# Optimization experiments

Hardware: AMD Instinct MI355X
Metric: run time of the kernel (lower is better)

Reference implementation:

```python
import jax, jax.numpy as jnp
import numpy as np

LATENT = 2048
PROJ = 128
N = 4096
TEMP = 0.5
BN_EPS = 1e-5
COS_EPS = 1e-8


def _batchnorm(x, gamma=None, beta=None):
    # training-mode BatchNorm1d: biased batch stats
    mean = jnp.mean(x, axis=0)
    var = jnp.mean((x - mean) ** 2, axis=0)
    xn = (x - mean) * jax.lax.rsqrt(var + BN_EPS)
    if gamma is not None:
        xn = xn * gamma + beta
    return xn


def _project(h, W1, gamma1, beta1, W2):
    x = h @ W1.T                      # [N, latent]
    x = jax.nn.relu(_batchnorm(x, gamma1, beta1))
    x = x @ W2.T                      # [N, proj]
    return _batchnorm(x)              # bn2 affine=False


def _normalize(z):
    n = jnp.linalg.norm(z, axis=-1, keepdims=True)
    return z / jnp.maximum(n, COS_EPS)


def setup_inputs() -> dict:
    key = jax.random.key(0)
    ks = jax.random.split(key, 4)
    scale_w1 = 1.0 / np.sqrt(LATENT)
    return {
        "h1": jax.random.normal(ks[0], (N, LATENT), jnp.float32),
        "h2": jax.random.normal(ks[1], (N, LATENT), jnp.float32),
        "W1": jax.random.normal(ks[2], (LATENT, LATENT), jnp.float32) * scale_w1,
        "gamma1": jnp.ones((LATENT,), jnp.float32),
        "beta1": jnp.zeros((LATENT,), jnp.float32),
        "W2": jax.random.normal(ks[3], (PROJ, LATENT), jnp.float32) * scale_w1,
    }


def reference(h1, h2, W1, gamma1, beta1, W2):
    z1 = _project(h1, W1, gamma1, beta1, W2)
    z2 = _project(h2, W1, gamma1, beta1, W2)
    zn1 = _normalize(z1)
    zn2 = _normalize(z2)
    inv_t = 1.0 / TEMP
    # cosine similarity as normalized GEMMs (same math as broadcast cossim)
    sim11 = (zn1 @ zn1.T) * inv_t      # [N, N]
    sim22 = (zn2 @ zn2.T) * inv_t
    sim12 = (zn1 @ zn2.T) * inv_t
    d = sim12.shape[-1]
    eye = jnp.eye(d, dtype=bool)
    neg_inf = jnp.float32(-jnp.inf)
    sim11 = jnp.where(eye, neg_inf, sim11)
    sim22 = jnp.where(eye, neg_inf, sim22)
    raw_scores1 = jnp.concatenate([sim12, sim11], axis=-1)       # [N, 2N]
    raw_scores2 = jnp.concatenate([sim22, sim12.T], axis=-1)     # [N, 2N]
    raw_scores = jnp.concatenate([raw_scores1, raw_scores2], axis=-2)  # [2N, 2N]
    targets = jnp.arange(2 * d, dtype=jnp.int64 if jax.config.jax_enable_x64 else jnp.int32)
    return raw_scores, targets
```

## Files before the change

### kernel.cpp

```cpp
#include <hip/hip_runtime.h>
#include <hip/hip_bf16.h>
#include <math.h>

#define NROWS 4096
#define MTOT  8192
#define LATENT 2048
#define PROJ 128
#define OUTN 8192
#define SPLITK 8
#define CH2 128

using bf16 = __hip_bfloat16;
using bf16x8 = __attribute__((ext_vector_type(8))) short;
using bf16x4 = __attribute__((ext_vector_type(4))) short;
using f32x4  = __attribute__((ext_vector_type(4))) float;

#define LDS_AS(p) ((__attribute__((address_space(3))) void*)(p))
#define GLB_AS(p) ((const __attribute__((address_space(1))) void*)(p))

__device__ __forceinline__ float bf2f(short s) {
    return __uint_as_float(((unsigned)(unsigned short)s) << 16);
}
__device__ __forceinline__ short f2bf(float f) {
    bf16 h = __float2bfloat16(f);
    return __builtin_bit_cast(short, h);
}

__global__ void conv_all(const float* __restrict__ W1, const float* __restrict__ W2,
                         const float* __restrict__ h1, const float* __restrict__ h2,
                         bf16* __restrict__ W1b, bf16* __restrict__ W2b,
                         bf16* __restrict__ hb)
{
    const size_t g = ((size_t)blockIdx.x * 256 + threadIdx.x) * 8;
    const size_t N_W1 = (size_t)LATENT * LATENT;
    const size_t N_W2 = (size_t)PROJ * LATENT;
    const size_t N_H  = (size_t)NROWS * LATENT;
    const float* src; bf16* dst; size_t off;
    if (g < N_W1)                  { src = W1; dst = W1b;       off = g; }
    else if (g < N_W1 + N_W2)      { src = W2; dst = W2b;       off = g - N_W1; }
    else if (g < N_W1 + N_W2 + N_H){ src = h1; dst = hb;        off = g - N_W1 - N_W2; }
    else                           { src = h2; dst = hb + N_H;  off = g - N_W1 - N_W2 - N_H; }
    const float4 v0 = *reinterpret_cast<const float4*>(src + off);
    const float4 v1 = *reinterpret_cast<const float4*>(src + off + 4);
    bf16x8 o;
    o[0] = f2bf(v0.x); o[1] = f2bf(v0.y); o[2] = f2bf(v0.z); o[3] = f2bf(v0.w);
    o[4] = f2bf(v1.x); o[5] = f2bf(v1.y); o[6] = f2bf(v1.z); o[7] = f2bf(v1.w);
    *reinterpret_cast<bf16x8*>(dst + off) = o;
}

#define AREG(buf,kh) (sm + ((buf)*2 + (kh)) * 16384)
#define BREG(buf,kh) (sm + 65536 + ((buf)*2 + (kh)) * 16384)

#define LDA_(buf,kh,m) (*reinterpret_cast<const bf16x8*>(AREG(buf,kh) + (wr*128 + (m)*16 + fr)*64 + rslot))
#define LDB_(buf,kh,n) (*reinterpret_cast<const bf16x8*>(BREG(buf,kh) + (wc*64  + (n)*16 + fr)*64 + rslot))

#define STAGE_A(buf,kh,kt) do { \
    const bf16* g_ = Ag + (size_t)(bm + w*16 + srow) * 2048 + (kt)*64 + (kh)*32 + selem; \
    __builtin_amdgcn_global_load_lds(GLB_AS(g_),                  LDS_AS(AREG(buf,kh) + w*1024),        16, 0, 0); \
    __builtin_amdgcn_global_load_lds(GLB_AS(g_ + (size_t)128*2048), LDS_AS(AREG(buf,kh) + 8192 + w*1024), 16, 0, 0); \
} while(0)

#define STAGE_B(buf,kh,kt) do { \
    const bf16* g_ = Bg + (size_t)(bn + w*16 + srow) * 2048 + (kt)*64 + (kh)*32 + selem; \
    __builtin_amdgcn_global_load_lds(GLB_AS(g_),                  LDS_AS(BREG(buf,kh) + w*1024),        16, 0, 0); \
    __builtin_amdgcn_global_load_lds(GLB_AS(g_ + (size_t)128*2048), LDS_AS(BREG(buf,kh) + 8192 + w*1024), 16, 0, 0); \
} while(0)

#define PH(bufi, khi, mb, READB, STAGE_STMT, DO_VMCNT) do { \
    if (READB) { b0 = LDB_(bufi,khi,0); b1 = LDB_(bufi,khi,1); b2 = LDB_(bufi,khi,2); b3 = LDB_(bufi,khi,3); } \
    bf16x8 a0 = LDA_(bufi,khi,(mb)+0), a1 = LDA_(bufi,khi,(mb)+1), a2 = LDA_(bufi,khi,(mb)+2), a3 = LDA_(bufi,khi,(mb)+3); \
    STAGE_STMT; \
    __builtin_amdgcn_s_barrier(); \
    asm volatile("s_waitcnt lgkmcnt(0)" ::: "memory"); \
    __builtin_amdgcn_sched_barrier(0); \
    __builtin_amdgcn_s_setprio(1); \
    acc[(mb)+0][0] = __builtin_amdgcn_mfma_f32_16x16x32_bf16(b0, a0, acc[(mb)+0][0], 0,0,0); \
    acc[(mb)+0][1] = __builtin_amdgcn_mfma_f32_16x16x32_bf16(b1, a0, acc[(mb)+0][1], 0,0,0); \
    acc[(mb)+0][2] = __builtin_amdgcn_mfma_f32_16x16x32_bf16(b2, a0, acc[(mb)+0][2], 0,0,0); \
    acc[(mb)+0][3] = __builtin_amdgcn_mfma_f32_16x16x32_bf16(b3, a0, acc[(mb)+0][3], 0,0,0); \
    acc[(mb)+1][0] = __builtin_amdgcn_mfma_f32_16x16x32_bf16(b0, a1, acc[(mb)+1][0], 0,0,0); \
    acc[(mb)+1][1] = __builtin_amdgcn_mfma_f32_16x16x32_bf16(b1, a1, acc[(mb)+1][1], 0,0,0); \
    acc[(mb)+1][2] = __builtin_amdgcn_mfma_f32_16x16x32_bf16(b2, a1, acc[(mb)+1][2], 0,0,0); \
    acc[(mb)+1][3] = __builtin_amdgcn_mfma_f32_16x16x32_bf16(b3, a1, acc[(mb)+1][3], 0,0,0); \
    acc[(mb)+2][0] = __builtin_amdgcn_mfma_f32_16x16x32_bf16(b0, a2, acc[(mb)+2][0], 0,0,0); \
    acc[(mb)+2][1] = __builtin_amdgcn_mfma_f32_16x16x32_bf16(b1, a2, acc[(mb)+2][1], 0,0,0); \
    acc[(mb)+2][2] = __builtin_amdgcn_mfma_f32_16x16x32_bf16(b2, a2, acc[(mb)+2][2], 0,0,0); \
    acc[(mb)+2][3] = __builtin_amdgcn_mfma_f32_16x16x32_bf16(b3, a2, acc[(mb)+2][3], 0,0,0); \
    acc[(mb)+3][0] = __builtin_amdgcn_mfma_f32_16x16x32_bf16(b0, a3, acc[(mb)+3][0], 0,0,0); \
    acc[(mb)+3][1] = __builtin_amdgcn_mfma_f32_16x16x32_bf16(b1, a3, acc[(mb)+3][1], 0,0,0); \
    acc[(mb)+3][2] = __builtin_amdgcn_mfma_f32_16x16x32_bf16(b2, a3, acc[(mb)+3][2], 0,0,0); \
    acc[(mb)+3][3] = __builtin_amdgcn_mfma_f32_16x16x32_bf16(b3, a3, acc[(mb)+3][3], 0,0,0); \
    __builtin_amdgcn_s_setprio(0); \
    if (DO_VMCNT) { asm volatile("s_waitcnt vmcnt(6)" ::: "memory"); } \
    __builtin_amdgcn_s_barrier(); \
    __builtin_amdgcn_sched_barrier(0); \
} while (0)

__global__ __launch_bounds__(512, 2)
void gemm1_256(const bf16* __restrict__ Ag, const bf16* __restrict__ Bg,
               bf16* __restrict__ C, float* __restrict__ pS1, float* __restrict__ pSS1)
{
    extern __shared__ __align__(16) char sm[];

    const int t    = threadIdx.x;
    const int lane = t & 63;
    const int w    = t >> 6;
    const int wr   = w >> 2;
    const int wc   = w & 3;

    const int bid = blockIdx.x;
    const int lin = (bid & 7) * 32 + (bid >> 3);
    const int bm  = (lin >> 3) * 256;
    const int bn  = (lin & 7) * 256;

    const int srow  = lane >> 2;
    const int selem = 8 * ((lane & 3) ^ ((lane >> 2) & 3));
    const int fr    = lane & 15;
    const int rslot = 16 * ((lane >> 4) ^ (lane & 3));

    f32x4 acc[8][4];
#pragma unroll
    for (int m = 0; m < 8; ++m)
#pragma unroll
        for (int n = 0; n < 4; ++n)
#pragma unroll
            for (int r = 0; r < 4; ++r) acc[m][n][r] = 0.f;

    bf16x8 b0, b1, b2, b3;

    STAGE_B(0,0,0); STAGE_A(0,0,0); STAGE_B(0,1,0); STAGE_A(0,1,0);
    STAGE_B(1,0,1); STAGE_A(1,0,1); STAGE_B(1,1,1);
    asm volatile("s_waitcnt vmcnt(6)" ::: "memory");
    __builtin_amdgcn_s_barrier();
    __builtin_amdgcn_sched_barrier(0);

    for (int i = 0; i < 15; ++i) {
        const int kt1 = 2*i + 1, kt2 = 2*i + 2, kt3 = 2*i + 3;
        PH(0,0, 0, true,  STAGE_A(1,1,kt1), false);
        PH(0,0, 4, false, STAGE_B(0,0,kt2), false);
        PH(0,1, 0, true,  STAGE_A(0,0,kt2), false);
        PH(0,1, 4, false, STAGE_B(0,1,kt2), true);
        PH(1,0, 0, true,  STAGE_A(0,1,kt2), false);
        PH(1,0, 4, false, STAGE_B(1,0,kt3), false);
        PH(1,1, 0, true,  STAGE_A(1,0,kt3), false);
        PH(1,1, 4, false, STAGE_B(1,1,kt3), true);
    }

    STAGE_A(1,1,31);
    asm volatile("s_waitcnt vmcnt(0)" ::: "memory");
    __builtin_amdgcn_s_barrier();
    __builtin_amdgcn_sched_barrier(0);
    PH(0,0, 0, true,  ((void)0), false);
    PH(0,0, 4, false, ((void)0), false);
    PH(0,1, 0, true,  ((void)0), false);
    PH(0,1, 4, false, ((void)0), false);
    PH(1,0, 0, true,  ((void)0), false);
    PH(1,0, 4, false, ((void)0), false);
    PH(1,1, 0, true,  ((void)0), false);
    PH(1,1, 4, false, ((void)0), false);

    const int j_l = (lane >> 4) * 4;
#pragma unroll
    for (int m = 0; m < 8; ++m)
#pragma unroll
        for (int n = 0; n < 4; ++n) {
            const int crow = bm + wr * 128 + m * 16 + fr;
            const int ccol = bn + wc * 64 + n * 16 + j_l;
            bf16x4 o;
#pragma unroll
            for (int r = 0; r < 4; ++r) o[r] = f2bf(acc[m][n][r]);
            *reinterpret_cast<bf16x4*>(&C[(size_t)crow * LATENT + ccol]) = o;
        }

#pragma unroll
    for (int n = 0; n < 4; ++n)
#pragma unroll
        for (int r = 0; r < 4; ++r) {
            float sv = 0.f, qv = 0.f;
#pragma unroll
            for (int m = 0; m < 8; ++m) {
                const float v = acc[m][n][r];
                sv += v;
                qv = fmaf(v, v, qv);
            }
#pragma unroll
            for (int o = 1; o < 16; o <<= 1) {
                sv += __shfl_xor(sv, o);
                qv += __shfl_xor(qv, o);
            }
            if (fr == 0) {
                const int slot = ((bm >> 8) << 1) + wr;
                const int col  = bn + wc * 64 + n * 16 + j_l + r;
                pS1 [(size_t)slot * LATENT + col] = sv;
                pSS1[(size_t)slot * LATENT + col] = qv;
            }
        }
}

__global__ void stats1_final(const float* __restrict__ pS, const float* __restrict__ pSS,
                             float* __restrict__ mean, float* __restrict__ rstd)
{
    const int c    = blockIdx.x * 256 + threadIdx.x;
    const int half = blockIdx.y;
    float s = 0.f, ss = 0.f;
    for (int i = 0; i < 32; ++i) {
        s  += pS [((size_t)(half * 32 + i)) * LATENT + c];
        ss += pSS[((size_t)(half * 32 + i)) * LATENT + c];
    }
    const float m   = s / NROWS;
    const float var = ss / NROWS - m * m;
    mean[half * LATENT + c] = m;
    rstd[half * LATENT + c] = 1.0f / sqrtf(var + 1e-5f);
}

__global__ void bn1_apply_relu_bf16(bf16* __restrict__ X,
                                    const float* __restrict__ mean, const float* __restrict__ rstd,
                                    const float* __restrict__ gamma, const float* __restrict__ beta)
{
    const size_t idx = (size_t)blockIdx.x * 256 + threadIdx.x;
    const size_t e   = idx * 8;
    const int c      = (int)(e & (LATENT - 1));
    const int half   = (int)(e >> 23);
    const int sc     = half * LATENT + c;
    const bf16x8 v = *reinterpret_cast<const bf16x8*>(X + e);
    const float4 m0 = *reinterpret_cast<const float4*>(mean + sc);
    const float4 m1 = *reinterpret_cast<const float4*>(mean + sc + 4);
    const float4 r0 = *reinterpret_cast<const float4*>(rstd + sc);
    const float4 r1 = *reinterpret_cast<const float4*>(rstd + sc + 4);
    const float4 g0 = *reinterpret_cast<const float4*>(gamma + c);
    const float4 g1 = *reinterpret_cast<const float4*>(gamma + c + 4);
    const float4 b0 = *reinterpret_cast<const float4*>(beta + c);
    const float4 b1 = *reinterpret_cast<const float4*>(beta + c + 4);
    const float mm[8] = {m0.x, m0.y, m0.z, m0.w, m1.x, m1.y, m1.z, m1.w};
    const float rr[8] = {r0.x, r0.y, r0.z, r0.w, r1.x, r1.y, r1.z, r1.w};
    const float gg[8] = {g0.x, g0.y, g0.z, g0.w, g1.x, g1.y, g1.z, g1.w};
    const float bb[8] = {b0.x, b0.y, b0.z, b0.w, b1.x, b1.y, b1.z, b1.w};
    bf16x8 o;
#pragma unroll
    for (int j = 0; j < 8; ++j) {
        const float f = fmaxf(fmaf((bf2f(v[j]) - mm[j]) * rr[j], gg[j], bb[j]), 0.f);
        o[j] = f2bf(f);
    }
    *reinterpret_cast<bf16x8*>(X + e) = o;
}

__global__ __launch_bounds__(256)
void gemm2_splitk(const bf16* __restrict__ A, const bf16* __restrict__ B,
                  float* __restrict__ Part)
{
    __shared__ __align__(16) bf16 As[128 * 32];
    __shared__ __align__(16) bf16 Bs[128 * 32];

    const int kc = blockIdx.x;
    const int bm = blockIdx.y * 128;

    const int t    = threadIdx.x;
    const int lane = t & 63;
    const int w    = t >> 6;
    const int wr   = w >> 1;
    const int wc   = w & 1;
    const int lrow = lane >> 2;
    const int lcol = (lane & 3) * 8;

    f32x4 acc[4][4];
#pragma unroll
    for (int m = 0; m < 4; ++m)
#pragma unroll
        for (int n = 0; n < 4; ++n)
#pragma unroll
            for (int r = 0; r < 4; ++r) acc[m][n][r] = 0.f;

    const int fr = lane & 15;
    const int fk = (lane >> 4) * 8;
    const int kbeg = kc * (LATENT / SPLITK);
    const int kend = kbeg + (LATENT / SPLITK);

    for (int k0 = kbeg; k0 < kend; k0 += 32) {
#pragma unroll
        for (int q = 0; q < 2; ++q) {
            const int chunk = w * 2 + q;
            const int row = chunk * 16 + lrow;
            __builtin_amdgcn_global_load_lds(
                GLB_AS(&A[(size_t)(bm + row) * LATENT + k0 + lcol]),
                LDS_AS(&As[chunk * 512]), 16, 0, 0);
            __builtin_amdgcn_global_load_lds(
                GLB_AS(&B[(size_t)row * LATENT + k0 + lcol]),
                LDS_AS(&Bs[chunk * 512]), 16, 0, 0);
        }
        __syncthreads();

        bf16x8 a[4], b[4];
#pragma unroll
        for (int m = 0; m < 4; ++m)
            a[m] = *reinterpret_cast<const bf16x8*>(&As[(wr * 64 + m * 16 + fr) * 32 + fk]);
#pragma unroll
        for (int n = 0; n < 4; ++n)
            b[n] = *reinterpret_cast<const bf16x8*>(&Bs[(wc * 64 + n * 16 + fr) * 32 + fk]);

#pragma unroll
        for (int m = 0; m < 4; ++m)
#pragma unroll
            for (int n = 0; n < 4; ++n)
                acc[m][n] = __builtin_amdgcn_mfma_f32_16x16x32_bf16(b[n], a[m], acc[m][n], 0, 0, 0);
        __syncthreads();
    }

    const int i_l = lane & 15;
    const int j_l = (lane >> 4) * 4;
#pragma unroll
    for (int m = 0; m < 4; ++m)
#pragma unroll
        for (int n = 0; n < 4; ++n) {
            const int crow = bm + wr * 64 + m * 16 + i_l;
            const int ccol = wc * 64 + n * 16 + j_l;
            *reinterpret_cast<float4*>(&Part[((size_t)kc * MTOT + crow) * PROJ + ccol]) =
                make_float4(acc[m][n][0], acc[m][n][1], acc[m][n][2], acc[m][n][3]);
        }
}

__global__ __launch_bounds__(128)
void reduce2_kern(const float* __restrict__ Part, float* __restrict__ Z,
                  float* __restrict__ pS2, float* __restrict__ pSS2)
{
    const int c     = threadIdx.x;
    const int chunk = blockIdx.x;
    const int r0    = chunk * (MTOT / CH2);
    float s = 0.f, ss = 0.f;
    for (int r = r0; r < r0 + MTOT / CH2; ++r) {
        float z = 0.f;
#pragma unroll
        for (int kc = 0; kc < SPLITK; ++kc)
            z += Part[((size_t)kc * MTOT + r) * PROJ + c];
        Z[(size_t)r * PROJ + c] = z;
        s += z;
        ss = fmaf(z, z, ss);
    }
    pS2 [(size_t)chunk * PROJ + c] = s;
    pSS2[(size_t)chunk * PROJ + c] = ss;
}

__global__ __launch_bounds__(128)
void stats2_final(const float* __restrict__ pS, const float* __restrict__ pSS,
                  float* __restrict__ mean, float* __restrict__ rstd)
{
    const int c    = threadIdx.x;
    const int half = blockIdx.x;
    float s = 0.f, ss = 0.f;
    for (int i = 0; i < CH2 / 2; ++i) {
        s  += pS [(size_t)(half * (CH2 / 2) + i) * PROJ + c];
        ss += pSS[(size_t)(half * (CH2 / 2) + i) * PROJ + c];
    }
    const float m   = s / NROWS;
    const float var = ss / NROWS - m * m;
    mean[half * PROJ + c] = m;
    rstd[half * PROJ + c] = 1.0f / sqrtf(var + 1e-5f);
}

__global__ __launch_bounds__(256)
void bn2_normalize_bf16(const float* __restrict__ Z,
                        const float* __restrict__ mean, const float* __restrict__ rstd,
                        bf16* __restrict__ Zn, int* __restrict__ tgt)
{
    const int row  = blockIdx.x * 4 + (threadIdx.x >> 6);
    const int half = row >> 12;
    const int lane = threadIdx.x & 63;
    const float* zr = Z + (size_t)row * PROJ;
    const float v0 = (zr[lane]      - mean[half * PROJ + lane])      * rstd[half * PROJ + lane];
    const float v1 = (zr[lane + 64] - mean[half * PROJ + lane + 64]) * rstd[half * PROJ + lane + 64];
    float ss = v0 * v0 + v1 * v1;
#pragma unroll
    for (int o = 32; o > 0; o >>= 1) ss += __shfl_xor(ss, o);
    const float inv = 1.0f / fmaxf(sqrtf(ss), 1e-8f);
    bf16* orow = Zn + (size_t)row * PROJ;
    orow[lane]      = __float2bfloat16(v0 * inv);
    orow[lane + 64] = __float2bfloat16(v1 * inv);
    if (lane == 0) tgt[row] = row;
}

__global__ __launch_bounds__(256)
void sim_bf16(const bf16* __restrict__ zn, float* __restrict__ out)
{
    __shared__ __align__(16) bf16 As[4 * 128 * 32];
    __shared__ __align__(16) bf16 Bs[4 * 128 * 32];

    const int t    = threadIdx.x;
    const int lane = t & 63;
    const int w    = t >> 6;
    const int wr   = w >> 1;
    const int wc   = w & 1;
    const int bi   = blockIdx.y * 128;
    const int bj   = blockIdx.x * 128;

    const bf16* Ub = zn + (size_t)bi * PROJ;
    const bf16* Vb = zn + (size_t)(bj ^ 4096) * PROJ;

    const int srow = t >> 2;
    const int ske  = (t & 3) * 8;

#pragma unroll
    for (int q = 0; q < 4; ++q)
#pragma unroll
        for (int h = 0; h < 2; ++h) {
            const int row = h * 64 + srow;
            const int ke  = q * 32 + ske;
            __builtin_amdgcn_global_load_lds(
                GLB_AS(&Ub[(size_t)row * PROJ + ke]),
                LDS_AS(&As[q * 4096 + h * 2048 + srow * 32 + ske]), 16, 0, 0);
            __builtin_amdgcn_global_load_lds(
                GLB_AS(&Vb[(size_t)row * PROJ + ke]),
                LDS_AS(&Bs[q * 4096 + h * 2048 + srow * 32 + ske]), 16, 0, 0);
        }
    __syncthreads();

    f32x4 acc[4][4];
#pragma unroll
    for (int m = 0; m < 4; ++m)
#pragma unroll
        for (int n = 0; n < 4; ++n)
#pragma unroll
            for (int r = 0; r < 4; ++r) acc[m][n][r] = 0.f;

    const int fr = lane & 15;
    const int fk = (lane >> 4) * 8;

#pragma unroll
    for (int q = 0; q < 4; ++q) {
        bf16x8 a[4], b[4];
#pragma unroll
        for (int m = 0; m < 4; ++m)
            a[m] = *reinterpret_cast<const bf16x8*>(&As[q * 4096 + (wr * 64 + m * 16 + fr) * 32 + fk]);
#pragma unroll
        for (int n = 0; n < 4; ++n)
            b[n] = *reinterpret_cast<const bf16x8*>(&Bs[q * 4096 + (wc * 64 + n * 16 + fr) * 32 + fk]);
#pragma unroll
        for (int m = 0; m < 4; ++m)
#pragma unroll
            for (int n = 0; n < 4; ++n)
                acc[m][n] = __builtin_amdgcn_mfma_f32_16x16x32_bf16(b[n], a[m], acc[m][n], 0, 0, 0);
    }

    const int i_l = lane & 15;
    const int j_l = (lane >> 4) * 4;
#pragma unroll
    for (int m = 0; m < 4; ++m)
#pragma unroll
        for (int n = 0; n < 4; ++n) {
            const int gi  = bi + wr * 64 + m * 16 + i_l;
            const int gj0 = bj + wc * 64 + n * 16 + j_l;
            f32x4 v;
#pragma unroll
            for (int r = 0; r < 4; ++r) v[r] = acc[m][n][r] * 2.0f;
            const int mj = (gi ^ 4096) - gj0;
            if (mj >= 0 && mj < 4) v[mj] = -1.0e30f;
            __builtin_nontemporal_store(
                v, reinterpret_cast<f32x4*>(&out[(size_t)gi * OUTN + gj0]));
        }
}

extern "C" void kernel_launch(void* const* d_in, const int* in_sizes, int n_in,
                              void* d_out, int out_size, void* d_ws, size_t ws_size,
                              hipStream_t stream)
{
    const float* h1 = (const float*)d_in[0];
    const float* h2 = (const float*)d_in[1];
    const float* W1 = (const float*)d_in[2];
    const float* g1 = (const float*)d_in[3];
    const float* b1 = (const float*)d_in[4];
    const float* W2 = (const float*)d_in[5];
    float* out = (float*)d_out;

    char* p = (char*)d_ws;
    auto carve = [&](size_t bytes) { char* r = p; p += (bytes + 255) & ~(size_t)255; return r; };
    bf16*  W1b   = (bf16*) carve((size_t)LATENT * LATENT * 2);
    bf16*  W2b   = (bf16*) carve((size_t)PROJ * LATENT * 2);
    bf16*  hb    = (bf16*) carve((size_t)MTOT * LATENT * 2);
    bf16*  X     = (bf16*) carve((size_t)MTOT * LATENT * 2);
    float* Part  = (float*)carve((size_t)SPLITK * MTOT * PROJ * 4);
    float* Z     = (float*)carve((size_t)MTOT * PROJ * 4);
    bf16*  znb   = (bf16*) carve((size_t)MTOT * PROJ * 2);
    float* pS1   = (float*)carve((size_t)64 * LATENT * 4);
    float* pSS1  = (float*)carve((size_t)64 * LATENT * 4);
    float* pS2   = (float*)carve((size_t)CH2 * PROJ * 4);
    float* pSS2  = (float*)carve((size_t)CH2 * PROJ * 4);
    float* mean1 = (float*)carve(2 * LATENT * 4);
    float* rstd1 = (float*)carve(2 * LATENT * 4);
    float* mean2 = (float*)carve(2 * PROJ * 4);
    float* rstd2 = (float*)carve(2 * PROJ * 4);

    const int conv_groups = (LATENT * LATENT + PROJ * LATENT + 2 * NROWS * LATENT) / 8;
    conv_all<<<dim3(conv_groups / 256), 256, 0, stream>>>(W1, W2, h1, h2, W1b, W2b, hb);

    gemm1_256<<<dim3(256), 512, 131072, stream>>>(hb, W1b, X, pS1, pSS1);

    stats1_final<<<dim3(LATENT / 256, 2), 256, 0, stream>>>(pS1, pSS1, mean1, rstd1);
    bn1_apply_relu_bf16<<<dim3(MTOT * LATENT / 2048), 256, 0, stream>>>(X, mean1, rstd1, g1, b1);

    gemm2_splitk<<<dim3(SPLITK, MTOT / 128), 256, 0, stream>>>(X, W2b, Part);
    reduce2_kern<<<dim3(CH2), 128, 0, stream>>>(Part, Z, pS2, pSS2);
    stats2_final<<<dim3(2), 128, 0, stream>>>(pS2, pSS2, mean2, rstd2);

    int* tgt = (int*)(out + (size_t)OUTN * OUTN);
    bn2_normalize_bf16<<<dim3(MTOT / 4), 256, 0, stream>>>(Z, mean2, rstd2, znb, tgt);

    sim_bf16<<<dim3(OUTN / 128, OUTN / 128), 256, 0, stream>>>(znb, out);
}
```

Measured before the change: 231.8 us.

## Fuse BN1 apply+ReLU into GEMM2 A-load and fold stats2 into normalize

```diff
diff --git a/kernel.cpp b/kernel.cpp
--- a/kernel.cpp
+++ b/kernel.cpp
@@ -198,7 +198,8 @@
 }
 
 __global__ void stats1_final(const float* __restrict__ pS, const float* __restrict__ pSS,
-                             float* __restrict__ mean, float* __restrict__ rstd)
+                             const float* __restrict__ gamma, const float* __restrict__ beta,
+                             float* __restrict__ scale1, float* __restrict__ shift1)
 {
     const int c    = blockIdx.x * 256 + threadIdx.x;
     const int half = blockIdx.y;
@@ -207,52 +208,25 @@
         s  += pS [((size_t)(half * 32 + i)) * LATENT + c];
         ss += pSS[((size_t)(half * 32 + i)) * LATENT + c];
     }
-    const float m   = s / NROWS;
-    const float var = ss / NROWS - m * m;
-    mean[half * LATENT + c] = m;
-    rstd[half * LATENT + c] = 1.0f / sqrtf(var + 1e-5f);
-}
-
-__global__ void bn1_apply_relu_bf16(bf16* __restrict__ X,
-                                    const float* __restrict__ mean, const float* __restrict__ rstd,
-                                    const float* __restrict__ gamma, const float* __restrict__ beta)
-{
-    const size_t idx = (size_t)blockIdx.x * 256 + threadIdx.x;
-    const size_t e   = idx * 8;
-    const int c      = (int)(e & (LATENT - 1));
-    const int half   = (int)(e >> 23);
-    const int sc     = half * LATENT + c;
-    const bf16x8 v = *reinterpret_cast<const bf16x8*>(X + e);
-    const float4 m0 = *reinterpret_cast<const float4*>(mean + sc);
-    const float4 m1 = *reinterpret_cast<const float4*>(mean + sc + 4);
-    const float4 r0 = *reinterpret_cast<const float4*>(rstd + sc);
-    const float4 r1 = *reinterpret_cast<const float4*>(rstd + sc + 4);
-    const float4 g0 = *reinterpret_cast<const float4*>(gamma + c);
-    const float4 g1 = *reinterpret_cast<const float4*>(gamma + c + 4);
-    const float4 b0 = *reinterpret_cast<const float4*>(beta + c);
-    const float4 b1 = *reinterpret_cast<const float4*>(beta + c + 4);
-    const float mm[8] = {m0.x, m0.y, m0.z, m0.w, m1.x, m1.y, m1.z, m1.w};
-    const float rr[8] = {r0.x, r0.y, r0.z, r0.w, r1.x, r1.y, r1.z, r1.w};
-    const float gg[8] = {g0.x, g0.y, g0.z, g0.w, g1.x, g1.y, g1.z, g1.w};
-    const float bb[8] = {b0.x, b0.y, b0.z, b0.w, b1.x, b1.y, b1.z, b1.w};
-    bf16x8 o;
-#pragma unroll
-    for (int j = 0; j < 8; ++j) {
-        const float f = fmaxf(fmaf((bf2f(v[j]) - mm[j]) * rr[j], gg[j], bb[j]), 0.f);
-        o[j] = f2bf(f);
-    }
-    *reinterpret_cast<bf16x8*>(X + e) = o;
+    const float m    = s / NROWS;
+    const float var  = ss / NROWS - m * m;
+    const float rstd = 1.0f / sqrtf(var + 1e-5f);
+    const float sc   = rstd * gamma[c];
+    scale1[half * LATENT + c] = sc;
+    shift1[half * LATENT + c] = beta[c] - m * sc;
 }
 
 __global__ __launch_bounds__(256)
-void gemm2_splitk(const bf16* __restrict__ A, const bf16* __restrict__ B,
-                  float* __restrict__ Part)
+void gemm2_fused(const bf16* __restrict__ A, const bf16* __restrict__ B,
+                 const float* __restrict__ scale1, const float* __restrict__ shift1,
+                 float* __restrict__ Part)
 {
     __shared__ __align__(16) bf16 As[128 * 32];
     __shared__ __align__(16) bf16 Bs[128 * 32];
 
     const int kc = blockIdx.x;
     const int bm = blockIdx.y * 128;
+    const int hb_ = (bm >> 12) * LATENT;
 
     const int t    = threadIdx.x;
     const int lane = t & 63;
@@ -281,11 +255,26 @@
             const int chunk = w * 2 + q;
             const int row = chunk * 16 + lrow;
             __builtin_amdgcn_global_load_lds(
-                GLB_AS(&A[(size_t)(bm + row) * LATENT + k0 + lcol]),
-                LDS_AS(&As[chunk * 512]), 16, 0, 0);
-            __builtin_amdgcn_global_load_lds(
                 GLB_AS(&B[(size_t)row * LATENT + k0 + lcol]),
                 LDS_AS(&Bs[chunk * 512]), 16, 0, 0);
+        }
+        const float4 sc0 = *reinterpret_cast<const float4*>(&scale1[hb_ + k0 + lcol]);
+        const float4 sc1 = *reinterpret_cast<const float4*>(&scale1[hb_ + k0 + lcol + 4]);
+        const float4 sh0 = *reinterpret_cast<const float4*>(&shift1[hb_ + k0 + lcol]);
+        const float4 sh1 = *reinterpret_cast<const float4*>(&shift1[hb_ + k0 + lcol + 4]);
+        const float scv[8] = {sc0.x, sc0.y, sc0.z, sc0.w, sc1.x, sc1.y, sc1.z, sc1.w};
+        const float shv[8] = {sh0.x, sh0.y, sh0.z, sh0.w, sh1.x, sh1.y, sh1.z, sh1.w};
+#pragma unroll
+        for (int q = 0; q < 2; ++q) {
+            const int chunk = w * 2 + q;
+            const int row = chunk * 16 + lrow;
+            const bf16x8 av = *reinterpret_cast<const bf16x8*>(
+                &A[(size_t)(bm + row) * LATENT + k0 + lcol]);
+            bf16x8 o;
+#pragma unroll
+            for (int j = 0; j < 8; ++j)
+                o[j] = f2bf(fmaxf(fmaf(bf2f(av[j]), scv[j], shv[j]), 0.f));
+            *reinterpret_cast<bf16x8*>(&As[chunk * 512 + lane * 8]) = o;
         }
         __syncthreads();
 
@@ -339,42 +328,49 @@
     pSS2[(size_t)chunk * PROJ + c] = ss;
 }
 
-__global__ __launch_bounds__(128)
-void stats2_final(const float* __restrict__ pS, const float* __restrict__ pSS,
-                  float* __restrict__ mean, float* __restrict__ rstd)
-{
-    const int c    = threadIdx.x;
-    const int half = blockIdx.x;
-    float s = 0.f, ss = 0.f;
-    for (int i = 0; i < CH2 / 2; ++i) {
-        s  += pS [(size_t)(half * (CH2 / 2) + i) * PROJ + c];
-        ss += pSS[(size_t)(half * (CH2 / 2) + i) * PROJ + c];
-    }
-    const float m   = s / NROWS;
-    const float var = ss / NROWS - m * m;
-    mean[half * PROJ + c] = m;
-    rstd[half * PROJ + c] = 1.0f / sqrtf(var + 1e-5f);
-}
-
 __global__ __launch_bounds__(256)
-void bn2_normalize_bf16(const float* __restrict__ Z,
-                        const float* __restrict__ mean, const float* __restrict__ rstd,
-                        bf16* __restrict__ Zn, int* __restrict__ tgt)
-{
-    const int row  = blockIdx.x * 4 + (threadIdx.x >> 6);
-    const int half = row >> 12;
-    const int lane = threadIdx.x & 63;
-    const float* zr = Z + (size_t)row * PROJ;
-    const float v0 = (zr[lane]      - mean[half * PROJ + lane])      * rstd[half * PROJ + lane];
-    const float v1 = (zr[lane + 64] - mean[half * PROJ + lane + 64]) * rstd[half * PROJ + lane + 64];
-    float ss = v0 * v0 + v1 * v1;
-#pragma unroll
-    for (int o = 32; o > 0; o >>= 1) ss += __shfl_xor(ss, o);
-    const float inv = 1.0f / fmaxf(sqrtf(ss), 1e-8f);
-    bf16* orow = Zn + (size_t)row * PROJ;
-    orow[lane]      = __float2bfloat16(v0 * inv);
-    orow[lane + 64] = __float2bfloat16(v1 * inv);
-    if (lane == 0) tgt[row] = row;
+void bn2_norm(const float* __restrict__ Z,
+              const float* __restrict__ pS2, const float* __restrict__ pSS2,
+              bf16* __restrict__ Zn, int* __restrict__ tgt)
+{
+    __shared__ float sm_mean[PROJ];
+    __shared__ float sm_rstd[PROJ];
+
+    const int blk  = blockIdx.x;
+    const int half = blk >> 5;
+    const int t    = threadIdx.x;
+
+    if (t < PROJ) {
+        float s = 0.f, ss = 0.f;
+        for (int i = 0; i < CH2 / 2; ++i) {
+            const int chunk = half * (CH2 / 2) + i;
+            s  += pS2 [(size_t)chunk * PROJ + t];
+            ss += pSS2[(size_t)chunk * PROJ + t];
+        }
+        const float m   = s / NROWS;
+        const float var = ss / NROWS - m * m;
+        sm_mean[t] = m;
+        sm_rstd[t] = 1.0f / sqrtf(var + 1e-5f);
+    }
+    __syncthreads();
+
+    const int lane = t & 63;
+    const int sub  = t >> 6;
+#pragma unroll 4
+    for (int it = 0; it < 32; ++it) {
+        const int row = blk * 128 + it * 4 + sub;
+        const float* zr = Z + (size_t)row * PROJ;
+        const float v0 = (zr[lane]      - sm_mean[lane])      * sm_rstd[lane];
+        const float v1 = (zr[lane + 64] - sm_mean[lane + 64]) * sm_rstd[lane + 64];
+        float ss = v0 * v0 + v1 * v1;
+#pragma unroll
+        for (int o = 32; o > 0; o >>= 1) ss += __shfl_xor(ss, o);
+        const float inv = 1.0f / fmaxf(sqrtf(ss), 1e-8f);
+        bf16* orow = Zn + (size_t)row * PROJ;
+        orow[lane]      = __float2bfloat16(v0 * inv);
+        orow[lane + 64] = __float2bfloat16(v1 * inv);
+        if (lane == 0) tgt[row] = row;
+    }
 }
 
 __global__ __launch_bounds__(256)
@@ -482,25 +478,22 @@
     float* pSS1  = (float*)carve((size_t)64 * LATENT * 4);
     float* pS2   = (float*)carve((size_t)CH2 * PROJ * 4);
     float* pSS2  = (float*)carve((size_t)CH2 * PROJ * 4);
-    float* mean1 = (float*)carve(2 * LATENT * 4);
-    float* rstd1 = (float*)carve(2 * LATENT * 4);
-    float* mean2 = (float*)carve(2 * PROJ * 4);
-    float* rstd2 = (float*)carve(2 * PROJ * 4);
+    float* scale1= (float*)carve(2 * LATENT * 4);
+    float* shift1= (float*)carve(2 * LATENT * 4);
 
     const int conv_groups = (LATENT * LATENT + PROJ * LATENT + 2 * NROWS * LATENT) / 8;
     conv_all<<<dim3(conv_groups / 256), 256, 0, stream>>>(W1, W2, h1, h2, W1b, W2b, hb);
 
     gemm1_256<<<dim3(256), 512, 131072, stream>>>(hb, W1b, X, pS1, pSS1);
 
-    stats1_final<<<dim3(LATENT / 256, 2), 256, 0, stream>>>(pS1, pSS1, mean1, rstd1);
-    bn1_apply_relu_bf16<<<dim3(MTOT * LATENT / 2048), 256, 0, stream>>>(X, mean1, rstd1, g1, b1);
-
-    gemm2_splitk<<<dim3(SPLITK, MTOT / 128), 256, 0, stream>>>(X, W2b, Part);
+    stats1_final<<<dim3(LATENT / 256, 2), 256, 0, stream>>>(pS1, pSS1, g1, b1, scale1, shift1);
+
+    gemm2_fused<<<dim3(SPLITK, MTOT / 128), 256, 0, stream>>>(X, W2b, scale1, shift1, Part);
+
     reduce2_kern<<<dim3(CH2), 128, 0, stream>>>(Part, Z, pS2, pSS2);
-    stats2_final<<<dim3(2), 128, 0, stream>>>(pS2, pSS2, mean2, rstd2);
 
     int* tgt = (int*)(out + (size_t)OUTN * OUTN);
-    bn2_normalize_bf16<<<dim3(MTOT / 4), 256, 0, stream>>>(Z, mean2, rstd2, znb, tgt);
+    bn2_norm<<<dim3(64), 256, 0, stream>>>(Z, pS2, pSS2, znb, tgt);
 
     sim_bf16<<<dim3(OUTN / 128, OUTN / 128), 256, 0, stream>>>(znb, out);
 }
```

Result: no change. 234.1 us (+1.0%).
